# Performance work log

Hardware: AMD Instinct MI355X
Metric: run time of the kernel (lower is better)

## Reference

```python
import jax, jax.numpy as jnp
import numpy as np

N_HEADS = 16
MASK_FILL = -2.0**15 + 1.0  # -32767, matches torch reference


def setup_inputs() -> dict:
    key = jax.random.key(0)
    ks = jax.random.split(key, 10)
    B, N, D = 4, 2048, 1024
    sc = 0.02
    return {
        "q": jax.random.normal(ks[0], (B, N, D), jnp.float32),
        "k": jax.random.normal(ks[1], (B, N, D), jnp.float32),
        "v": jax.random.normal(ks[2], (B, N, D), jnp.float32),
        "Wq": jax.random.normal(ks[3], (D, D), jnp.float32) * sc,
        "bq": jnp.zeros((D,), jnp.float32),
        "Wk": jax.random.normal(ks[4], (D, D), jnp.float32) * sc,
        "bk": jnp.zeros((D,), jnp.float32),
        "Wv": jax.random.normal(ks[5], (D, D), jnp.float32) * sc,
        "bv": jnp.zeros((D,), jnp.float32),
        "Wo": jax.random.normal(ks[6], (D, D), jnp.float32) * sc,
    }


def reference(q, k, v, Wq, bq, Wk, bk, Wv, bv, Wo):
    B, N, D = q.shape
    H = N_HEADS
    dh = D // H
    scale = dh ** (-0.5)

    def proj(x, W, b):
        # torch nn.Linear: x @ W.T + b, W stored as (out, in)
        y = jnp.einsum('bnd,od->bno', x, W) + b
        return y.reshape(B, N, H, dh).transpose(0, 2, 1, 3)  # b h n d

    qh = proj(q, Wq, bq)
    kh = proj(k, Wk, bk)
    vh = proj(v, Wv, bv)

    scores = jnp.einsum('bhnd,bhmd->bhnm', qh, kh) * scale  # [B,H,N,N]
    causal = jnp.tril(jnp.ones((N, N), dtype=bool))
    scores = jnp.where(causal, scores, jnp.float32(MASK_FILL))
    attn = jax.nn.softmax(scores, axis=-1)
    x = jnp.einsum('bhnm,bhmd->bhnd', attn, vh)
    x = x.transpose(0, 2, 1, 3).reshape(B, N, D)  # b n (h d)
    return jnp.einsum('bnd,od->bno', x, Wo)  # to_out Linear, bias=False; dropout p=0
```

## Files before the change

### kernel.cpp

```cpp
#include <hip/hip_runtime.h>
#include <hip/hip_bf16.h>
#include <cstdint>
#include <cstddef>

typedef __bf16 bf16_t;
typedef __bf16 bf16x4 __attribute__((ext_vector_type(4)));
typedef __bf16 bf16x8 __attribute__((ext_vector_type(8)));
typedef float  f32x4  __attribute__((ext_vector_type(4)));

static constexpr int Bsz  = 4;
static constexpr int Nseq = 2048;
static constexpr int Dmod = 1024;
static constexpr int H    = 16;
static constexpr int DH   = 64;
static constexpr int M_TOT = Bsz * Nseq;
static constexpr int K    = 1024;
static constexpr int BM = 128, BN = 128, BK = 32;

#define WAITVM(N) asm volatile("s_waitcnt vmcnt(" #N ")" ::: "memory")

__device__ __forceinline__ f32x4 mfma16(bf16x8 a, bf16x8 b, f32x4 c) {
  return __builtin_amdgcn_mfma_f32_16x16x32_bf16(a, b, c, 0, 0, 0);
}

__device__ __forceinline__ bf16x8 cvt8(const float* p) {
  f32x4 lo = *(const f32x4*)(p);
  f32x4 hi = *(const f32x4*)(p + 4);
  bf16x8 r;
#pragma unroll
  for (int i = 0; i < 4; ++i) { r[i] = (bf16_t)lo[i]; r[4 + i] = (bf16_t)hi[i]; }
  return r;
}

__device__ __forceinline__ void async16(const bf16_t* g, bf16_t* l) {
  __builtin_amdgcn_global_load_lds(
      (const __attribute__((address_space(1))) void*)g,
      (__attribute__((address_space(3))) void*)l, 16, 0, 0);
}

struct CvtArgs {
  const float* src[7];
  bf16_t* dst[7];
  int n[7];
};

__global__ __launch_bounds__(256) void cvt_kernel(CvtArgs a) {
  const int z = blockIdx.y;
  const float* s = a.src[z];
  bf16x8* d = (bf16x8*)a.dst[z];
  const int n8 = a.n[z] >> 3;
  const int stride = gridDim.x * 256;
  for (int i = blockIdx.x * 256 + threadIdx.x; i < n8; i += stride)
    d[i] = cvt8(s + (size_t)i * 8);
}

template <int MODE, typename CT>
__device__ __forceinline__ void gemm_body(
    bf16_t (*As)[BM][BK], bf16_t (*Ws)[BN][BK],
    const bf16_t* __restrict__ A, const bf16_t* __restrict__ W,
    const float* __restrict__ bias, CT* __restrict__ C, float oscale) {
  const int tid  = threadIdx.x;
  const int lane = tid & 63;
  const int wave = tid >> 6;
  const int wm = wave & 1, wn = wave >> 1;
  const int row = lane & 15, quad = lane >> 4;

  const int m_blk = blockIdx.x * BM;
  const int n_blk = blockIdx.y * BN;

  f32x4 acc[4][4];
#pragma unroll
  for (int i = 0; i < 4; ++i)
#pragma unroll
    for (int j = 0; j < 4; ++j) acc[i][j] = (f32x4){0.f, 0.f, 0.f, 0.f};

  const int srow = lane >> 2;
  const int scol = (lane & 3) * 8;

  const bf16_t* Abase = A + (size_t)m_blk * K + scol;
  const bf16_t* Wbase = W + (size_t)n_blk * K + scol;

  constexpr int NT = K / BK;

  auto stage = [&](int t, int buf) {
#pragma unroll
    for (int j = 0; j < 2; ++j) {
      const int seg = wave * 2 + j;
      async16(Abase + (size_t)(seg * 16 + srow) * K + t * BK,
              &As[buf][seg * 16][0]);
      async16(Wbase + (size_t)(seg * 16 + srow) * K + t * BK,
              &Ws[buf][seg * 16][0]);
    }
  };

  stage(0, 0);
  stage(1, 1);
  int buf = 0, bufn = 2;

#pragma unroll 1
  for (int it = 0; it < NT; ++it) {
    if (it + 1 < NT) { WAITVM(4); } else { WAITVM(0); }
    __builtin_amdgcn_s_barrier();

    bf16x8 af[4], wf[4];
#pragma unroll
    for (int i = 0; i < 4; ++i)
      af[i] = *(const bf16x8*)(&As[buf][wm * 64 + i * 16 + row][quad * 8]);
#pragma unroll
    for (int i = 0; i < 4; ++i)
      wf[i] = *(const bf16x8*)(&Ws[buf][wn * 64 + i * 16 + row][quad * 8]);

    if (it + 2 < NT) stage(it + 2, bufn);

#pragma unroll
    for (int i = 0; i < 4; ++i)
#pragma unroll
      for (int j = 0; j < 4; ++j) {
        if (MODE == 1)
          acc[i][j] = mfma16(af[i], wf[j], acc[i][j]);
        else
          acc[i][j] = mfma16(wf[j], af[i], acc[i][j]);
      }

    buf  = (buf  == 2) ? 0 : buf  + 1;
    bufn = (bufn == 2) ? 0 : bufn + 1;
  }

  if (MODE == 0) {
#pragma unroll
    for (int i = 0; i < 4; ++i) {
      const int m = m_blk + wm * 64 + i * 16 + row;
      const int b = m >> 11, n = m & 2047;
#pragma unroll
      for (int j = 0; j < 4; ++j) {
        const int o0 = n_blk + wn * 64 + j * 16 + quad * 4;
        const int hh = o0 >> 6, od = o0 & 63;
        const f32x4 bv4 = *(const f32x4*)(bias + o0);
        const size_t idx0 = (((size_t)b * H + hh) * Nseq + n) * DH + od;
        bf16x4 pkt;
#pragma unroll
        for (int r = 0; r < 4; ++r)
          pkt[r] = (bf16_t)((acc[i][j][r] + bv4[r]) * oscale);
        *(bf16x4*)((bf16_t*)C + idx0) = pkt;
      }
    }
  } else if (MODE == 2) {
#pragma unroll
    for (int i = 0; i < 4; ++i) {
      const int m = m_blk + wm * 64 + i * 16 + row;
#pragma unroll
      for (int j = 0; j < 4; ++j) {
        const int o0 = n_blk + wn * 64 + j * 16 + quad * 4;
        *(f32x4*)((float*)C + (size_t)m * Dmod + o0) = acc[i][j];
      }
    }
  } else {
#pragma unroll
    for (int j = 0; j < 4; ++j) {
      const int o = n_blk + wn * 64 + j * 16 + row;
      const float bv = bias[o];
      const int hh = o >> 6, od = o & 63;
#pragma unroll
      for (int i = 0; i < 4; ++i) {
        const int m0 = m_blk + wm * 64 + i * 16 + quad * 4;
        const int b = m0 >> 11, n = m0 & 2047;
        const size_t idx0 = (((size_t)b * H + hh) * DH + od) * Nseq + n;
        bf16x4 pkt;
#pragma unroll
        for (int r = 0; r < 4; ++r)
          pkt[r] = (bf16_t)(acc[i][j][r] + bv);
        *(bf16x4*)((bf16_t*)C + idx0) = pkt;
      }
    }
  }
}

struct QkvArgs {
  const bf16_t* A[3];
  const bf16_t* W[3];
  const float*  bias[3];
  bf16_t*       out[3];
};

__global__ __launch_bounds__(256) void qkv_gemm(QkvArgs a, float qscale) {
  __shared__ bf16_t As[3][BM][BK];
  __shared__ bf16_t Ws[3][BN][BK];
  const int z = blockIdx.z;
  if (z == 2)
    gemm_body<1, bf16_t>(As, Ws, a.A[2], a.W[2], a.bias[2], a.out[2], 1.f);
  else if (z == 1)
    gemm_body<0, bf16_t>(As, Ws, a.A[1], a.W[1], a.bias[1], a.out[1], 1.f);
  else
    gemm_body<0, bf16_t>(As, Ws, a.A[0], a.W[0], a.bias[0], a.out[0], qscale);
}

__global__ __launch_bounds__(256) void out_gemm(
    const bf16_t* __restrict__ A, const bf16_t* __restrict__ W,
    float* __restrict__ C) {
  __shared__ bf16_t As[3][BM][BK];
  __shared__ bf16_t Ws[3][BN][BK];
  gemm_body<2, float>(As, Ws, A, W, nullptr, C, 1.f);
}

__global__ __launch_bounds__(256, 4) void attn_fwd(
    const bf16_t* __restrict__ Q, const bf16_t* __restrict__ Kh,
    const bf16_t* __restrict__ VT, bf16_t* __restrict__ X) {
  const int lane = threadIdx.x & 63;
  const int wave = threadIdx.x >> 6;
  const int bid = blockIdx.x;
  const int bh = (bid & 7) * 8 + ((bid >> 3) & 7);
  const int qt = 31 - (bid >> 6);
  const int b = bh >> 4, h = bh & 15;
  const int row = lane & 15, quad = lane >> 4;

  __shared__ __align__(16) bf16_t Kt[3][32][64];
  __shared__ __align__(16) bf16_t Vt[3][64][32];
  __shared__ __align__(16) bf16_t plds[4][16][56];

  const bf16_t* Qb = Q + (size_t)bh * Nseq * DH;
  const bf16_t* Kb = Kh + (size_t)bh * Nseq * DH;
  const bf16_t* Vb = VT + (size_t)bh * DH * Nseq;

  const int krow_l = lane >> 3;
  const int kc8    = lane & 7;
  const bf16_t* ksrc =
      Kb + (size_t)(wave * 8 + krow_l) * DH + (kc8 ^ krow_l) * 8;
  bf16_t* kdst = &Kt[0][wave * 8][0];

  const int vd_l = lane >> 2;
  const int vkc  = lane & 3;
  const int vd   = wave * 16 + vd_l;
  const bf16_t* vsrc =
      Vb + (size_t)vd * Nseq + (vkc ^ ((vd_l >> 1) & 3)) * 8;
  bf16_t* vdst = &Vt[0][wave * 16][0];

  auto stage = [&](int t, int buf) {
    async16(ksrc + (size_t)t * (32 * DH), kdst + buf * (32 * 64));
    async16(vsrc + t * 32, vdst + buf * (64 * 32));
  };

  const int q0 = qt * 64 + wave * 16;
  const int qg = q0 + row;

  bf16x8 qf0 = *(const bf16x8*)(Qb + (size_t)(q0 + row) * DH + quad * 8);
  bf16x8 qf1 = *(const bf16x8*)(Qb + (size_t)(q0 + row) * DH + 32 + quad * 8);

  f32x4 o_acc[4];
#pragma unroll
  for (int c = 0; c < 4; ++c) o_acc[c] = (f32x4){0.f, 0.f, 0.f, 0.f};
  f32x4 lsv = (f32x4){0.f, 0.f, 0.f, 0.f};

  const int nfull = 2 * qt;
  const int NT = nfull + 2;

  auto read_kf = [&](bf16x8 (&kf)[2][2], int bf) {
#pragma unroll
    for (int c = 0; c < 2; ++c)
#pragma unroll
      for (int hf = 0; hf < 2; ++hf)
        kf[c][hf] = *(const bf16x8*)(
            &Kt[bf][c * 16 + row][((hf * 4 + quad) ^ (row & 7)) * 8]);
  };
  auto read_vf = [&](bf16x8 (&vf)[4], int bf) {
#pragma unroll
    for (int ch = 0; ch < 4; ++ch)
      vf[ch] = *(const bf16x8*)(
          &Vt[bf][ch * 16 + row][(quad ^ ((row >> 1) & 3)) * 8]);
  };
  auto qk = [&](f32x4 (&s)[2], const bf16x8 (&kf)[2][2]) {
    __builtin_amdgcn_s_setprio(1);
#pragma unroll
    for (int c = 0; c < 2; ++c) {
      s[c] = (f32x4){0.f, 0.f, 0.f, 0.f};
      s[c] = mfma16(kf[c][0], qf0, s[c]);
      s[c] = mfma16(kf[c][1], qf1, s[c]);
    }
    __builtin_amdgcn_s_setprio(0);
  };
  auto pv = [&](const bf16x8& pf, const bf16x8 (&vf)[4]) {
    __builtin_amdgcn_s_setprio(1);
#pragma unroll
    for (int ch = 0; ch < 4; ++ch)
      o_acc[ch] = mfma16(pf, vf[ch], o_acc[ch]);
    __builtin_amdgcn_s_setprio(0);
  };
  auto softmax_store = [&](const f32x4 (&s)[2], int it, bf16x8& pfN) {
    const bool mask = (it >= nfull);
    const int k0 = it * 32;
#pragma unroll
    for (int c = 0; c < 2; ++c) {
      bf16x4 pk;
      f32x4 pv4;
#pragma unroll
      for (int r = 0; r < 4; ++r) {
        float t = s[c][r];
        if (mask) {
          const int kg = k0 + c * 16 + quad * 4 + r;
          t = (kg <= qg) ? t : -1e38f;
        }
        float p = __builtin_amdgcn_exp2f(t);
        pv4[r] = p;
        pk[r] = (bf16_t)p;
      }
      lsv += pv4;
      *(bf16x4*)(&plds[wave][row][c * 16 + quad * 4]) = pk;
    }
    asm volatile("" ::: "memory");
    pfN = *(const bf16x8*)(&plds[wave][row][quad * 8]);
  };

  bf16x8 vfA[4], vfB[4], pfA, pfB;

  stage(0, 0);
  stage(1, 1);

  {
    WAITVM(2);
    __builtin_amdgcn_s_barrier();
    bf16x8 kf[2][2];
    read_kf(kf, 0);
    read_vf(vfA, 0);
    if (NT > 2) stage(2, 2);
    f32x4 s[2];
    qk(s, kf);
    softmax_store(s, 0, pfA);
  }

  int buf = 1, bufn = (NT > 2) ? 0 : 2;

#pragma unroll 1
  for (int it = 1; it + 1 < NT; it += 2) {
    {
      WAITVM(2);
      __builtin_amdgcn_s_barrier();
      bf16x8 kf[2][2];
      read_kf(kf, buf);
      read_vf(vfB, buf);
      if (it + 2 < NT) stage(it + 2, bufn);
      f32x4 s[2];
      qk(s, kf);
      pv(pfA, vfA);
      softmax_store(s, it, pfB);
      buf  = (buf  == 2) ? 0 : buf  + 1;
      bufn = (bufn == 2) ? 0 : bufn + 1;
    }
    {
      WAITVM(2);
      __builtin_amdgcn_s_barrier();
      bf16x8 kf[2][2];
      read_kf(kf, buf);
      read_vf(vfA, buf);
      if (it + 3 < NT) stage(it + 3, bufn);
      f32x4 s[2];
      qk(s, kf);
      pv(pfB, vfB);
      softmax_store(s, it + 1, pfA);
      buf  = (buf  == 2) ? 0 : buf  + 1;
      bufn = (bufn == 2) ? 0 : bufn + 1;
    }
  }

  {
    WAITVM(0);
    __builtin_amdgcn_s_barrier();
    bf16x8 kf[2][2];
    read_kf(kf, buf);
    read_vf(vfB, buf);
    f32x4 s[2];
    qk(s, kf);
    pv(pfA, vfA);
    softmax_store(s, NT - 1, pfB);
  }
  pv(pfB, vfB);

  float ls = (lsv[0] + lsv[1]) + (lsv[2] + lsv[3]);
  ls += __shfl_xor(ls, 16, 64);
  ls += __shfl_xor(ls, 32, 64);

#pragma unroll
  for (int r = 0; r < 4; ++r) {
    const float linv = 1.f / __shfl(ls, quad * 4 + r, 64);
    const int qq = q0 + quad * 4 + r;
    const size_t base = ((size_t)b * Nseq + qq) * Dmod + h * DH;
#pragma unroll
    for (int ch = 0; ch < 4; ++ch)
      X[base + ch * 16 + row] = (bf16_t)(o_acc[ch][r] * linv);
  }
}

extern "C" void kernel_launch(void* const* d_in, const int* in_sizes, int n_in,
                              void* d_out, int out_size, void* d_ws,
                              size_t ws_size, hipStream_t stream) {
  const float* q  = (const float*)d_in[0];
  const float* k  = (const float*)d_in[1];
  const float* v  = (const float*)d_in[2];
  const float* Wq = (const float*)d_in[3];
  const float* bq = (const float*)d_in[4];
  const float* Wk = (const float*)d_in[5];
  const float* bk = (const float*)d_in[6];
  const float* Wv = (const float*)d_in[7];
  const float* bv = (const float*)d_in[8];
  const float* Wo = (const float*)d_in[9];
  float* out = (float*)d_out;

  const size_t E  = (size_t)M_TOT * Dmod;
  const size_t EW = (size_t)Dmod * Dmod;
  bf16_t* ws = (bf16_t*)d_ws;
  bf16_t* qb  = ws;
  bf16_t* kb  = ws + E;
  bf16_t* vb  = ws + 2 * E;
  bf16_t* Wqb = ws + 3 * E;
  bf16_t* Wkb = Wqb + EW;
  bf16_t* Wvb = Wkb + EW;
  bf16_t* Wob = Wvb + EW;
  bf16_t* Qh  = Wob + EW;
  bf16_t* Kh  = Qh + E;
  bf16_t* VT  = Kh + E;
  bf16_t* X   = kb;

  CvtArgs ca;
  ca.src[0] = q;  ca.dst[0] = qb;  ca.n[0] = (int)E;
  ca.src[1] = k;  ca.dst[1] = kb;  ca.n[1] = (int)E;
  ca.src[2] = v;  ca.dst[2] = vb;  ca.n[2] = (int)E;
  ca.src[3] = Wq; ca.dst[3] = Wqb; ca.n[3] = (int)EW;
  ca.src[4] = Wk; ca.dst[4] = Wkb; ca.n[4] = (int)EW;
  ca.src[5] = Wv; ca.dst[5] = Wvb; ca.n[5] = (int)EW;
  ca.src[6] = Wo; ca.dst[6] = Wob; ca.n[6] = (int)EW;
  cvt_kernel<<<dim3(512, 7), 256, 0, stream>>>(ca);

  const float C_SC = 0.125f * 1.44269504088896f;

  dim3 blk(256);
  QkvArgs qa;
  qa.A[0] = qb; qa.W[0] = Wqb; qa.bias[0] = bq; qa.out[0] = Qh;
  qa.A[1] = kb; qa.W[1] = Wkb; qa.bias[1] = bk; qa.out[1] = Kh;
  qa.A[2] = vb; qa.W[2] = Wvb; qa.bias[2] = bv; qa.out[2] = VT;
  qkv_gemm<<<dim3(M_TOT / BM, Dmod / BN, 3), blk, 0, stream>>>(qa, C_SC);

  attn_fwd<<<dim3(2048), blk, 0, stream>>>(Qh, Kh, VT, X);

  out_gemm<<<dim3(M_TOT / BM, Dmod / BN), blk, 0, stream>>>(X, Wob, out);
}
```

Baseline: 312.1 us.

## Replace 128x128 GEMMs with 256x256-tile, 8-wave ping-pong pipelined GEMM

Rewrites the QKV and output projection GEMMs to use 256x256 output tiles with 512 threads, BK=64, a double-buffered swizzled LDS layout, and an 8-phase schedule that interleaves async global->LDS loads with MFMA sub-blocks. The goal is more data reuse per loaded byte and global loads hidden behind compute. The cost is fewer blocks: the grid drops to 32x4x3 and 32x4, which risks underfilling the 256 CUs for out_gemm. It also adds higher register pressure and more barriers.

```diff
diff --git a/kernel.cpp b/kernel.cpp
--- a/kernel.cpp
+++ b/kernel.cpp
@@ -15,7 +15,6 @@
 static constexpr int DH   = 64;
 static constexpr int M_TOT = Bsz * Nseq;
 static constexpr int K    = 1024;
-static constexpr int BM = 128, BN = 128, BK = 32;
 
 #define WAITVM(N) asm volatile("s_waitcnt vmcnt(" #N ")" ::: "memory")
 
@@ -55,85 +54,211 @@
 }
 
 template <int MODE, typename CT>
-__device__ __forceinline__ void gemm_body(
-    bf16_t (*As)[BM][BK], bf16_t (*Ws)[BN][BK],
+__device__ __forceinline__ void gemm256_body(
+    bf16_t (*As)[2][128][64], bf16_t (*Bs)[2][128][64],
     const bf16_t* __restrict__ A, const bf16_t* __restrict__ W,
     const float* __restrict__ bias, CT* __restrict__ C, float oscale) {
   const int tid  = threadIdx.x;
   const int lane = tid & 63;
   const int wave = tid >> 6;
-  const int wm = wave & 1, wn = wave >> 1;
+  const int wr = wave >> 2;
+  const int wc = wave & 3;
   const int row = lane & 15, quad = lane >> 4;
-
-  const int m_blk = blockIdx.x * BM;
-  const int n_blk = blockIdx.y * BN;
-
-  f32x4 acc[4][4];
-#pragma unroll
-  for (int i = 0; i < 4; ++i)
+  const int m_blk = blockIdx.x * 256;
+  const int n_blk = blockIdx.y * 256;
+
+  f32x4 acc[8][4];
+#pragma unroll
+  for (int i = 0; i < 8; ++i)
 #pragma unroll
     for (int j = 0; j < 4; ++j) acc[i][j] = (f32x4){0.f, 0.f, 0.f, 0.f};
 
-  const int srow = lane >> 2;
-  const int scol = (lane & 3) * 8;
-
-  const bf16_t* Abase = A + (size_t)m_blk * K + scol;
-  const bf16_t* Wbase = W + (size_t)n_blk * K + scol;
-
-  constexpr int NT = K / BK;
-
-  auto stage = [&](int t, int buf) {
-#pragma unroll
-    for (int j = 0; j < 2; ++j) {
-      const int seg = wave * 2 + j;
-      async16(Abase + (size_t)(seg * 16 + srow) * K + t * BK,
-              &As[buf][seg * 16][0]);
-      async16(Wbase + (size_t)(seg * 16 + srow) * K + t * BK,
-              &Ws[buf][seg * 16][0]);
-    }
-  };
-
-  stage(0, 0);
-  stage(1, 1);
-  int buf = 0, bufn = 2;
+  auto stageA = [&](int t, int half) {
+#pragma unroll
+    for (int j2 = 0; j2 < 2; ++j2) {
+      const int l = j2 * 512 + wave * 64 + lane;
+      const int r = l >> 3;
+      const int cb = (l & 7) * 16;
+      const int cbs = cb ^ (((r >> 2) & 1) << 5);
+      async16(A + (size_t)(m_blk + half * 128 + r) * K + t * 64 + (cbs >> 1),
+              &As[t & 1][half][0][0] + (size_t)(wave * 64 + j2 * 512) * 8);
+    }
+  };
+  auto stageB = [&](int t, int half) {
+#pragma unroll
+    for (int j2 = 0; j2 < 2; ++j2) {
+      const int l = j2 * 512 + wave * 64 + lane;
+      const int r = l >> 3;
+      const int cb = (l & 7) * 16;
+      const int cbs = cb ^ (((r >> 2) & 1) << 5);
+      async16(W + (size_t)(n_blk + half * 128 + r) * K + t * 64 + (cbs >> 1),
+              &Bs[t & 1][half][0][0] + (size_t)(wave * 64 + j2 * 512) * 8);
+    }
+  };
+
+  auto rdA = [&](int slot, int fi, int ks) -> bf16x8 {
+    const int hrow = fi * 16 + row;
+    const int ke = (ks * 32 + quad * 8) ^ (((hrow >> 2) & 1) << 4);
+    return *(const bf16x8*)(&As[slot][wr][hrow][ke]);
+  };
+  auto rdB = [&](int slot, int fj, int ks) -> bf16x8 {
+    const int br = wc * 64 + fj * 16 + row;
+    const int hrow = br & 127;
+    const int ke = (ks * 32 + quad * 8) ^ (((hrow >> 2) & 1) << 4);
+    return *(const bf16x8*)(&Bs[slot][br >> 7][hrow][ke]);
+  };
+
+  bf16x8 af[4][2], bf[4][2];
+
+  auto MM = [&](int i, int j, const bf16x8& a8, const bf16x8& b8) {
+    if (MODE == 1) acc[i][j] = mfma16(a8, b8, acc[i][j]);
+    else           acc[i][j] = mfma16(b8, a8, acc[i][j]);
+  };
+
+#define PH_SYNC()                                            \
+  do {                                                       \
+    __builtin_amdgcn_s_barrier();                            \
+    asm volatile("s_waitcnt lgkmcnt(0)" ::: "memory");       \
+    __builtin_amdgcn_sched_barrier(0);                       \
+  } while (0)
+
+  constexpr int NTILE = K / 64;
+  constexpr int NI = NTILE / 2;
+
+  stageA(0, 0); stageA(0, 1); stageB(0, 0); stageB(0, 1);
+  stageB(1, 0); stageB(1, 1);
+  WAITVM(4);
+  __builtin_amdgcn_s_barrier();
 
 #pragma unroll 1
-  for (int it = 0; it < NT; ++it) {
-    if (it + 1 < NT) { WAITVM(4); } else { WAITVM(0); }
-    __builtin_amdgcn_s_barrier();
-
-    bf16x8 af[4], wf[4];
-#pragma unroll
-    for (int i = 0; i < 4; ++i)
-      af[i] = *(const bf16x8*)(&As[buf][wm * 64 + i * 16 + row][quad * 8]);
-#pragma unroll
-    for (int i = 0; i < 4; ++i)
-      wf[i] = *(const bf16x8*)(&Ws[buf][wn * 64 + i * 16 + row][quad * 8]);
-
-    if (it + 2 < NT) stage(it + 2, bufn);
-
-#pragma unroll
-    for (int i = 0; i < 4; ++i)
+  for (int i = 0; i < NI; ++i) {
+    const int t1 = 2 * i + 1, nt0 = 2 * i + 2, nt1 = 2 * i + 3;
+    const bool nl = (i + 1 < NI);
+
+#pragma unroll
+    for (int fi = 0; fi < 4; ++fi) { af[fi][0] = rdA(0, fi, 0); af[fi][1] = rdA(0, fi, 1); }
+#pragma unroll
+    for (int fj = 0; fj < 2; ++fj) { bf[fj][0] = rdB(0, fj, 0); bf[fj][1] = rdB(0, fj, 1); }
+    stageA(t1, 0);
+    PH_SYNC();
+    __builtin_amdgcn_s_setprio(1);
+#pragma unroll
+    for (int fi = 0; fi < 4; ++fi)
+#pragma unroll
+      for (int fj = 0; fj < 2; ++fj)
+#pragma unroll
+        for (int ks = 0; ks < 2; ++ks) MM(fi, fj, af[fi][ks], bf[fj][ks]);
+    __builtin_amdgcn_s_setprio(0);
+    __builtin_amdgcn_s_barrier();
+
+#pragma unroll
+    for (int fj = 2; fj < 4; ++fj) { bf[fj][0] = rdB(0, fj, 0); bf[fj][1] = rdB(0, fj, 1); }
+    stageA(t1, 1);
+    PH_SYNC();
+    __builtin_amdgcn_s_setprio(1);
+#pragma unroll
+    for (int fi = 0; fi < 4; ++fi)
+#pragma unroll
+      for (int fj = 2; fj < 4; ++fj)
+#pragma unroll
+        for (int ks = 0; ks < 2; ++ks) MM(fi, fj, af[fi][ks], bf[fj][ks]);
+    __builtin_amdgcn_s_setprio(0);
+    __builtin_amdgcn_s_barrier();
+
+#pragma unroll
+    for (int fi = 0; fi < 4; ++fi) { af[fi][0] = rdA(0, 4 + fi, 0); af[fi][1] = rdA(0, 4 + fi, 1); }
+    if (nl) stageB(nt0, 0);
+    PH_SYNC();
+    __builtin_amdgcn_s_setprio(1);
+#pragma unroll
+    for (int fi = 0; fi < 4; ++fi)
+#pragma unroll
+      for (int fj = 0; fj < 2; ++fj)
+#pragma unroll
+        for (int ks = 0; ks < 2; ++ks) MM(4 + fi, fj, af[fi][ks], bf[fj][ks]);
+    __builtin_amdgcn_s_setprio(0);
+    __builtin_amdgcn_s_barrier();
+
+    if (nl) stageB(nt0, 1);
+    PH_SYNC();
+    __builtin_amdgcn_s_setprio(1);
+#pragma unroll
+    for (int fi = 0; fi < 4; ++fi)
+#pragma unroll
+      for (int fj = 2; fj < 4; ++fj)
+#pragma unroll
+        for (int ks = 0; ks < 2; ++ks) MM(4 + fi, fj, af[fi][ks], bf[fj][ks]);
+    __builtin_amdgcn_s_setprio(0);
+    if (nl) { WAITVM(4); } else { WAITVM(0); }
+    __builtin_amdgcn_s_barrier();
+
+#pragma unroll
+    for (int fi = 0; fi < 4; ++fi) { af[fi][0] = rdA(1, fi, 0); af[fi][1] = rdA(1, fi, 1); }
+#pragma unroll
+    for (int fj = 0; fj < 2; ++fj) { bf[fj][0] = rdB(1, fj, 0); bf[fj][1] = rdB(1, fj, 1); }
+    if (nl) stageA(nt0, 0);
+    PH_SYNC();
+    __builtin_amdgcn_s_setprio(1);
+#pragma unroll
+    for (int fi = 0; fi < 4; ++fi)
+#pragma unroll
+      for (int fj = 0; fj < 2; ++fj)
+#pragma unroll
+        for (int ks = 0; ks < 2; ++ks) MM(fi, fj, af[fi][ks], bf[fj][ks]);
+    __builtin_amdgcn_s_setprio(0);
+    __builtin_amdgcn_s_barrier();
+
+#pragma unroll
+    for (int fj = 2; fj < 4; ++fj) { bf[fj][0] = rdB(1, fj, 0); bf[fj][1] = rdB(1, fj, 1); }
+    if (nl) stageA(nt0, 1);
+    PH_SYNC();
+    __builtin_amdgcn_s_setprio(1);
+#pragma unroll
+    for (int fi = 0; fi < 4; ++fi)
+#pragma unroll
+      for (int fj = 2; fj < 4; ++fj)
+#pragma unroll
+        for (int ks = 0; ks < 2; ++ks) MM(fi, fj, af[fi][ks], bf[fj][ks]);
+    __builtin_amdgcn_s_setprio(0);
+    __builtin_amdgcn_s_barrier();
+
+#pragma unroll
+    for (int fi = 0; fi < 4; ++fi) { af[fi][0] = rdA(1, 4 + fi, 0); af[fi][1] = rdA(1, 4 + fi, 1); }
+    if (nl) stageB(nt1, 0);
+    PH_SYNC();
+    __builtin_amdgcn_s_setprio(1);
+#pragma unroll
+    for (int fi = 0; fi < 4; ++fi)
+#pragma unroll
+      for (int fj = 0; fj < 2; ++fj)
+#pragma unroll
+        for (int ks = 0; ks < 2; ++ks) MM(4 + fi, fj, af[fi][ks], bf[fj][ks]);
+    __builtin_amdgcn_s_setprio(0);
+    __builtin_amdgcn_s_barrier();
+
+    if (nl) stageB(nt1, 1);
+    PH_SYNC();
+    __builtin_amdgcn_s_setprio(1);
+#pragma unroll
+    for (int fi = 0; fi < 4; ++fi)
+#pragma unroll
+      for (int fj = 2; fj < 4; ++fj)
+#pragma unroll
+        for (int ks = 0; ks < 2; ++ks) MM(4 + fi, fj, af[fi][ks], bf[fj][ks]);
+    __builtin_amdgcn_s_setprio(0);
+    if (nl) { WAITVM(4); } else { WAITVM(0); }
+    __builtin_amdgcn_s_barrier();
+  }
+#undef PH_SYNC
+
+  if (MODE == 0) {
+#pragma unroll
+    for (int i = 0; i < 8; ++i) {
+      const int m = m_blk + wr * 128 + i * 16 + row;
+      const int b = m >> 11, n = m & 2047;
 #pragma unroll
       for (int j = 0; j < 4; ++j) {
-        if (MODE == 1)
-          acc[i][j] = mfma16(af[i], wf[j], acc[i][j]);
-        else
-          acc[i][j] = mfma16(wf[j], af[i], acc[i][j]);
-      }
-
-    buf  = (buf  == 2) ? 0 : buf  + 1;
-    bufn = (bufn == 2) ? 0 : bufn + 1;
-  }
-
-  if (MODE == 0) {
-#pragma unroll
-    for (int i = 0; i < 4; ++i) {
-      const int m = m_blk + wm * 64 + i * 16 + row;
-      const int b = m >> 11, n = m & 2047;
-#pragma unroll
-      for (int j = 0; j < 4; ++j) {
-        const int o0 = n_blk + wn * 64 + j * 16 + quad * 4;
+        const int o0 = n_blk + wc * 64 + j * 16 + quad * 4;
         const int hh = o0 >> 6, od = o0 & 63;
         const f32x4 bv4 = *(const f32x4*)(bias + o0);
         const size_t idx0 = (((size_t)b * H + hh) * Nseq + n) * DH + od;
@@ -146,23 +271,23 @@
     }
   } else if (MODE == 2) {
 #pragma unroll
-    for (int i = 0; i < 4; ++i) {
-      const int m = m_blk + wm * 64 + i * 16 + row;
+    for (int i = 0; i < 8; ++i) {
+      const int m = m_blk + wr * 128 + i * 16 + row;
 #pragma unroll
       for (int j = 0; j < 4; ++j) {
-        const int o0 = n_blk + wn * 64 + j * 16 + quad * 4;
+        const int o0 = n_blk + wc * 64 + j * 16 + quad * 4;
         *(f32x4*)((float*)C + (size_t)m * Dmod + o0) = acc[i][j];
       }
     }
   } else {
 #pragma unroll
     for (int j = 0; j < 4; ++j) {
-      const int o = n_blk + wn * 64 + j * 16 + row;
+      const int o = n_blk + wc * 64 + j * 16 + row;
       const float bv = bias[o];
       const int hh = o >> 6, od = o & 63;
 #pragma unroll
-      for (int i = 0; i < 4; ++i) {
-        const int m0 = m_blk + wm * 64 + i * 16 + quad * 4;
+      for (int i = 0; i < 8; ++i) {
+        const int m0 = m_blk + wr * 128 + i * 16 + quad * 4;
         const int b = m0 >> 11, n = m0 & 2047;
         const size_t idx0 = (((size_t)b * H + hh) * DH + od) * Nseq + n;
         bf16x4 pkt;
@@ -182,24 +307,24 @@
   bf16_t*       out[3];
 };
 
-__global__ __launch_bounds__(256) void qkv_gemm(QkvArgs a, float qscale) {
-  __shared__ bf16_t As[3][BM][BK];
-  __shared__ bf16_t Ws[3][BN][BK];
+__global__ __launch_bounds__(512, 2) void qkv_gemm(QkvArgs a, float qscale) {
+  __shared__ __align__(16) bf16_t As[2][2][128][64];
+  __shared__ __align__(16) bf16_t Bs[2][2][128][64];
   const int z = blockIdx.z;
   if (z == 2)
-    gemm_body<1, bf16_t>(As, Ws, a.A[2], a.W[2], a.bias[2], a.out[2], 1.f);
+    gemm256_body<1, bf16_t>(As, Bs, a.A[2], a.W[2], a.bias[2], a.out[2], 1.f);
   else if (z == 1)
-    gemm_body<0, bf16_t>(As, Ws, a.A[1], a.W[1], a.bias[1], a.out[1], 1.f);
+    gemm256_body<0, bf16_t>(As, Bs, a.A[1], a.W[1], a.bias[1], a.out[1], 1.f);
   else
-    gemm_body<0, bf16_t>(As, Ws, a.A[0], a.W[0], a.bias[0], a.out[0], qscale);
-}
-
-__global__ __launch_bounds__(256) void out_gemm(
+    gemm256_body<0, bf16_t>(As, Bs, a.A[0], a.W[0], a.bias[0], a.out[0], qscale);
+}
+
+__global__ __launch_bounds__(512, 2) void out_gemm(
     const bf16_t* __restrict__ A, const bf16_t* __restrict__ W,
     float* __restrict__ C) {
-  __shared__ bf16_t As[3][BM][BK];
-  __shared__ bf16_t Ws[3][BN][BK];
-  gemm_body<2, float>(As, Ws, A, W, nullptr, C, 1.f);
+  __shared__ __align__(16) bf16_t As[2][2][128][64];
+  __shared__ __align__(16) bf16_t Bs[2][2][128][64];
+  gemm256_body<2, float>(As, Bs, A, W, nullptr, C, 1.f);
 }
 
 __global__ __launch_bounds__(256, 4) void attn_fwd(
@@ -253,19 +378,19 @@
   const int nfull = 2 * qt;
   const int NT = nfull + 2;
 
-  auto read_kf = [&](bf16x8 (&kf)[2][2], int bf) {
+  auto read_kf = [&](bf16x8 (&kf)[2][2], int bfv) {
 #pragma unroll
     for (int c = 0; c < 2; ++c)
 #pragma unroll
       for (int hf = 0; hf < 2; ++hf)
         kf[c][hf] = *(const bf16x8*)(
-            &Kt[bf][c * 16 + row][((hf * 4 + quad) ^ (row & 7)) * 8]);
-  };
-  auto read_vf = [&](bf16x8 (&vf)[4], int bf) {
+            &Kt[bfv][c * 16 + row][((hf * 4 + quad) ^ (row & 7)) * 8]);
+  };
+  auto read_vf = [&](bf16x8 (&vf)[4], int bfv) {
 #pragma unroll
     for (int ch = 0; ch < 4; ++ch)
       vf[ch] = *(const bf16x8*)(
-          &Vt[bf][ch * 16 + row][(quad ^ ((row >> 1) & 3)) * 8]);
+          &Vt[bfv][ch * 16 + row][(quad ^ ((row >> 1) & 3)) * 8]);
   };
   auto qk = [&](f32x4 (&s)[2], const bf16x8 (&kf)[2][2]) {
     __builtin_amdgcn_s_setprio(1);
@@ -430,14 +555,13 @@
 
   const float C_SC = 0.125f * 1.44269504088896f;
 
-  dim3 blk(256);
   QkvArgs qa;
   qa.A[0] = qb; qa.W[0] = Wqb; qa.bias[0] = bq; qa.out[0] = Qh;
   qa.A[1] = kb; qa.W[1] = Wkb; qa.bias[1] = bk; qa.out[1] = Kh;
   qa.A[2] = vb; qa.W[2] = Wvb; qa.bias[2] = bv; qa.out[2] = VT;
-  qkv_gemm<<<dim3(M_TOT / BM, Dmod / BN, 3), blk, 0, stream>>>(qa, C_SC);
-
-  attn_fwd<<<dim3(2048), blk, 0, stream>>>(Qh, Kh, VT, X);
-
-  out_gemm<<<dim3(M_TOT / BM, Dmod / BN), blk, 0, stream>>>(X, Wob, out);
-}
+  qkv_gemm<<<dim3(M_TOT / 256, Dmod / 256, 3), dim3(512), 0, stream>>>(qa, C_SC);
+
+  attn_fwd<<<dim3(2048), dim3(256), 0, stream>>>(Qh, Kh, VT, X);
+
+  out_gemm<<<dim3(M_TOT / 256, Dmod / 256), dim3(512), 0, stream>>>(X, Wob, out);
+}
```

Measured after the change: 333.6 us. 6.9% more time.

## Fuse fp32-to-bf16 activation conversion into QKV GEMM loads with swizzled LDS

Applied to the files above, without the earlier changes.

The separate conversion pass over the q/k/v activations is removed. The QKV GEMM now streams fp32 activations straight into LDS and converts them to bf16 when reading fragments, so only the weights are pre-converted. The GEMM pipeline also changes from triple to double buffering, adds an XOR swizzle to the LDS layout to reduce bank conflicts, and raises wave priority around the MFMA block. In exchange, the QKV GEMM moves twice as many A bytes per tile, re-converts each A element once per column block, and uses more LDS.

```diff
diff --git a/kernel.cpp b/kernel.cpp
--- a/kernel.cpp
+++ b/kernel.cpp
@@ -32,86 +32,118 @@
   return r;
 }
 
-__device__ __forceinline__ void async16(const bf16_t* g, bf16_t* l) {
+__device__ __forceinline__ void async16(const void* g, void* l) {
   __builtin_amdgcn_global_load_lds(
       (const __attribute__((address_space(1))) void*)g,
       (__attribute__((address_space(3))) void*)l, 16, 0, 0);
 }
 
 struct CvtArgs {
-  const float* src[7];
-  bf16_t* dst[7];
-  int n[7];
+  const float* src[4];
+  bf16_t* dst[4];
+  int n;
 };
 
 __global__ __launch_bounds__(256) void cvt_kernel(CvtArgs a) {
   const int z = blockIdx.y;
   const float* s = a.src[z];
   bf16x8* d = (bf16x8*)a.dst[z];
-  const int n8 = a.n[z] >> 3;
+  const int n8 = a.n >> 3;
   const int stride = gridDim.x * 256;
   for (int i = blockIdx.x * 256 + threadIdx.x; i < n8; i += stride)
     d[i] = cvt8(s + (size_t)i * 8);
 }
 
-template <int MODE, typename CT>
-__device__ __forceinline__ void gemm_body(
-    bf16_t (*As)[BM][BK], bf16_t (*Ws)[BN][BK],
-    const bf16_t* __restrict__ A, const bf16_t* __restrict__ W,
+template <int MODE, bool AF32, typename CT>
+__device__ __forceinline__ void gemm_body2(
+    void* AsRaw, bf16_t* Ws,
+    const void* Av, const bf16_t* __restrict__ W,
     const float* __restrict__ bias, CT* __restrict__ C, float oscale) {
   const int tid  = threadIdx.x;
   const int lane = tid & 63;
   const int wave = tid >> 6;
   const int wm = wave & 1, wn = wave >> 1;
   const int row = lane & 15, quad = lane >> 4;
-
   const int m_blk = blockIdx.x * BM;
   const int n_blk = blockIdx.y * BN;
 
+  float*  AsF = (float*)AsRaw;
+  bf16_t* AsB = (bf16_t*)AsRaw;
+  const float*  Af = (const float*)Av;
+  const bf16_t* Ab = (const bf16_t*)Av;
+
   f32x4 acc[4][4];
 #pragma unroll
   for (int i = 0; i < 4; ++i)
 #pragma unroll
     for (int j = 0; j < 4; ++j) acc[i][j] = (f32x4){0.f, 0.f, 0.f, 0.f};
 
-  const int srow = lane >> 2;
-  const int scol = (lane & 3) * 8;
-
-  const bf16_t* Abase = A + (size_t)m_blk * K + scol;
-  const bf16_t* Wbase = W + (size_t)n_blk * K + scol;
+  auto stageA = [&](int t, int s) {
+    if constexpr (AF32) {
+#pragma unroll
+      for (int j = 0; j < 4; ++j) {
+        const int g = (j * 4 + wave) * 64 + lane;
+        const int r = g >> 3, c = g & 7;
+        async16(Af + (size_t)(m_blk + r) * K + t * BK + ((c ^ (r & 7)) * 4),
+                AsF + s * 4096 + (j * 4 + wave) * 256);
+      }
+    } else {
+#pragma unroll
+      for (int j = 0; j < 2; ++j) {
+        const int g = (j * 4 + wave) * 64 + lane;
+        const int r = g >> 2, c = g & 3;
+        async16(Ab + (size_t)(m_blk + r) * K + t * BK + ((c ^ (r & 3)) * 8),
+                AsB + s * 4096 + (j * 4 + wave) * 512);
+      }
+    }
+  };
+  auto stageW = [&](int t, int s) {
+#pragma unroll
+    for (int j = 0; j < 2; ++j) {
+      const int g = (j * 4 + wave) * 64 + lane;
+      const int r = g >> 2, c = g & 3;
+      async16(W + (size_t)(n_blk + r) * K + t * BK + ((c ^ (r & 3)) * 8),
+              Ws + s * 4096 + (j * 4 + wave) * 512);
+    }
+  };
+
+  auto rdA = [&](int s, int i) -> bf16x8 {
+    const int hr = wm * 64 + i * 16 + row;
+    if constexpr (AF32) {
+      const float* bp = AsF + s * 4096 + hr * 32;
+      f32x4 lo = *(const f32x4*)(bp + (((2 * quad) ^ (hr & 7)) * 4));
+      f32x4 hi = *(const f32x4*)(bp + (((2 * quad + 1) ^ (hr & 7)) * 4));
+      bf16x8 o;
+#pragma unroll
+      for (int e = 0; e < 4; ++e) { o[e] = (bf16_t)lo[e]; o[4 + e] = (bf16_t)hi[e]; }
+      return o;
+    } else {
+      return *(const bf16x8*)(AsB + s * 4096 + hr * 32 + (quad ^ (hr & 3)) * 8);
+    }
+  };
+  auto rdW = [&](int s, int i) -> bf16x8 {
+    const int hr = wn * 64 + i * 16 + row;
+    return *(const bf16x8*)(Ws + s * 4096 + hr * 32 + (quad ^ (hr & 3)) * 8);
+  };
 
   constexpr int NT = K / BK;
 
-  auto stage = [&](int t, int buf) {
-#pragma unroll
-    for (int j = 0; j < 2; ++j) {
-      const int seg = wave * 2 + j;
-      async16(Abase + (size_t)(seg * 16 + srow) * K + t * BK,
-              &As[buf][seg * 16][0]);
-      async16(Wbase + (size_t)(seg * 16 + srow) * K + t * BK,
-              &Ws[buf][seg * 16][0]);
-    }
-  };
-
-  stage(0, 0);
-  stage(1, 1);
-  int buf = 0, bufn = 2;
+  stageA(0, 0); stageW(0, 0);
+  WAITVM(0);
+  __builtin_amdgcn_s_barrier();
 
 #pragma unroll 1
   for (int it = 0; it < NT; ++it) {
-    if (it + 1 < NT) { WAITVM(4); } else { WAITVM(0); }
-    __builtin_amdgcn_s_barrier();
+    const int s = it & 1;
+    if (it + 1 < NT) { stageA(it + 1, s ^ 1); stageW(it + 1, s ^ 1); }
 
     bf16x8 af[4], wf[4];
 #pragma unroll
-    for (int i = 0; i < 4; ++i)
-      af[i] = *(const bf16x8*)(&As[buf][wm * 64 + i * 16 + row][quad * 8]);
-#pragma unroll
-    for (int i = 0; i < 4; ++i)
-      wf[i] = *(const bf16x8*)(&Ws[buf][wn * 64 + i * 16 + row][quad * 8]);
-
-    if (it + 2 < NT) stage(it + 2, bufn);
-
+    for (int i = 0; i < 4; ++i) af[i] = rdA(s, i);
+#pragma unroll
+    for (int i = 0; i < 4; ++i) wf[i] = rdW(s, i);
+
+    __builtin_amdgcn_s_setprio(1);
 #pragma unroll
     for (int i = 0; i < 4; ++i)
 #pragma unroll
@@ -121,9 +153,9 @@
         else
           acc[i][j] = mfma16(wf[j], af[i], acc[i][j]);
       }
-
-    buf  = (buf  == 2) ? 0 : buf  + 1;
-    bufn = (bufn == 2) ? 0 : bufn + 1;
+    __builtin_amdgcn_s_setprio(0);
+    if (it + 1 < NT) WAITVM(0);
+    __builtin_amdgcn_s_barrier();
   }
 
   if (MODE == 0) {
@@ -176,30 +208,33 @@
 }
 
 struct QkvArgs {
-  const bf16_t* A[3];
+  const float*  A[3];
   const bf16_t* W[3];
   const float*  bias[3];
   bf16_t*       out[3];
 };
 
 __global__ __launch_bounds__(256) void qkv_gemm(QkvArgs a, float qscale) {
-  __shared__ bf16_t As[3][BM][BK];
-  __shared__ bf16_t Ws[3][BN][BK];
+  __shared__ __align__(16) float  AsF[2][128][32];
+  __shared__ __align__(16) bf16_t Ws2[2][128][32];
   const int z = blockIdx.z;
   if (z == 2)
-    gemm_body<1, bf16_t>(As, Ws, a.A[2], a.W[2], a.bias[2], a.out[2], 1.f);
+    gemm_body2<1, true, bf16_t>(AsF, &Ws2[0][0][0], a.A[2], a.W[2], a.bias[2],
+                                a.out[2], 1.f);
   else if (z == 1)
-    gemm_body<0, bf16_t>(As, Ws, a.A[1], a.W[1], a.bias[1], a.out[1], 1.f);
+    gemm_body2<0, true, bf16_t>(AsF, &Ws2[0][0][0], a.A[1], a.W[1], a.bias[1],
+                                a.out[1], 1.f);
   else
-    gemm_body<0, bf16_t>(As, Ws, a.A[0], a.W[0], a.bias[0], a.out[0], qscale);
+    gemm_body2<0, true, bf16_t>(AsF, &Ws2[0][0][0], a.A[0], a.W[0], a.bias[0],
+                                a.out[0], qscale);
 }
 
 __global__ __launch_bounds__(256) void out_gemm(
     const bf16_t* __restrict__ A, const bf16_t* __restrict__ W,
     float* __restrict__ C) {
-  __shared__ bf16_t As[3][BM][BK];
-  __shared__ bf16_t Ws[3][BN][BK];
-  gemm_body<2, float>(As, Ws, A, W, nullptr, C, 1.f);
+  __shared__ __align__(16) bf16_t AsB[2][128][32];
+  __shared__ __align__(16) bf16_t Ws2[2][128][32];
+  gemm_body2<2, false, float>(AsB, &Ws2[0][0][0], A, W, nullptr, C, 1.f);
 }
 
 __global__ __launch_bounds__(256, 4) void attn_fwd(
@@ -253,19 +288,19 @@
   const int nfull = 2 * qt;
   const int NT = nfull + 2;
 
-  auto read_kf = [&](bf16x8 (&kf)[2][2], int bf) {
+  auto read_kf = [&](bf16x8 (&kf)[2][2], int bfv) {
 #pragma unroll
     for (int c = 0; c < 2; ++c)
 #pragma unroll
       for (int hf = 0; hf < 2; ++hf)
         kf[c][hf] = *(const bf16x8*)(
-            &Kt[bf][c * 16 + row][((hf * 4 + quad) ^ (row & 7)) * 8]);
-  };
-  auto read_vf = [&](bf16x8 (&vf)[4], int bf) {
+            &Kt[bfv][c * 16 + row][((hf * 4 + quad) ^ (row & 7)) * 8]);
+  };
+  auto read_vf = [&](bf16x8 (&vf)[4], int bfv) {
 #pragma unroll
     for (int ch = 0; ch < 4; ++ch)
       vf[ch] = *(const bf16x8*)(
-          &Vt[bf][ch * 16 + row][(quad ^ ((row >> 1) & 3)) * 8]);
+          &Vt[bfv][ch * 16 + row][(quad ^ ((row >> 1) & 3)) * 8]);
   };
   auto qk = [&](f32x4 (&s)[2], const bf16x8 (&kf)[2][2]) {
     __builtin_amdgcn_s_setprio(1);
@@ -406,38 +441,32 @@
   const size_t E  = (size_t)M_TOT * Dmod;
   const size_t EW = (size_t)Dmod * Dmod;
   bf16_t* ws = (bf16_t*)d_ws;
-  bf16_t* qb  = ws;
-  bf16_t* kb  = ws + E;
-  bf16_t* vb  = ws + 2 * E;
-  bf16_t* Wqb = ws + 3 * E;
+  bf16_t* Wqb = ws;
   bf16_t* Wkb = Wqb + EW;
   bf16_t* Wvb = Wkb + EW;
   bf16_t* Wob = Wvb + EW;
   bf16_t* Qh  = Wob + EW;
   bf16_t* Kh  = Qh + E;
   bf16_t* VT  = Kh + E;
-  bf16_t* X   = kb;
+  bf16_t* X   = VT + E;
 
   CvtArgs ca;
-  ca.src[0] = q;  ca.dst[0] = qb;  ca.n[0] = (int)E;
-  ca.src[1] = k;  ca.dst[1] = kb;  ca.n[1] = (int)E;
-  ca.src[2] = v;  ca.dst[2] = vb;  ca.n[2] = (int)E;
-  ca.src[3] = Wq; ca.dst[3] = Wqb; ca.n[3] = (int)EW;
-  ca.src[4] = Wk; ca.dst[4] = Wkb; ca.n[4] = (int)EW;
-  ca.src[5] = Wv; ca.dst[5] = Wvb; ca.n[5] = (int)EW;
-  ca.src[6] = Wo; ca.dst[6] = Wob; ca.n[6] = (int)EW;
-  cvt_kernel<<<dim3(512, 7), 256, 0, stream>>>(ca);
+  ca.src[0] = Wq; ca.dst[0] = Wqb;
+  ca.src[1] = Wk; ca.dst[1] = Wkb;
+  ca.src[2] = Wv; ca.dst[2] = Wvb;
+  ca.src[3] = Wo; ca.dst[3] = Wob;
+  ca.n = (int)EW;
+  cvt_kernel<<<dim3(256, 4), 256, 0, stream>>>(ca);
 
   const float C_SC = 0.125f * 1.44269504088896f;
 
-  dim3 blk(256);
   QkvArgs qa;
-  qa.A[0] = qb; qa.W[0] = Wqb; qa.bias[0] = bq; qa.out[0] = Qh;
-  qa.A[1] = kb; qa.W[1] = Wkb; qa.bias[1] = bk; qa.out[1] = Kh;
-  qa.A[2] = vb; qa.W[2] = Wvb; qa.bias[2] = bv; qa.out[2] = VT;
-  qkv_gemm<<<dim3(M_TOT / BM, Dmod / BN, 3), blk, 0, stream>>>(qa, C_SC);
-
-  attn_fwd<<<dim3(2048), blk, 0, stream>>>(Qh, Kh, VT, X);
-
-  out_gemm<<<dim3(M_TOT / BM, Dmod / BN), blk, 0, stream>>>(X, Wob, out);
-}
+  qa.A[0] = q; qa.W[0] = Wqb; qa.bias[0] = bq; qa.out[0] = Qh;
+  qa.A[1] = k; qa.W[1] = Wkb; qa.bias[1] = bk; qa.out[1] = Kh;
+  qa.A[2] = v; qa.W[2] = Wvb; qa.bias[2] = bv; qa.out[2] = VT;
+  qkv_gemm<<<dim3(M_TOT / BM, Dmod / BN, 3), dim3(256), 0, stream>>>(qa, C_SC);
+
+  attn_fwd<<<dim3(2048), dim3(256), 0, stream>>>(Qh, Kh, VT, X);
+
+  out_gemm<<<dim3(M_TOT / BM, Dmod / BN), dim3(256), 0, stream>>>(X, Wob, out);
+}
```

Result: slower. 343.2 us (+10.0%).
